# Kernel optimization log

Hardware: AMD Instinct MI355X
Metric: run time of the kernel (lower is better)

## Reference

```python
import jax, jax.numpy as jnp
import numpy as np

B, T, C, H = 8, 2048, 1024, 64  # batch, seq (== block_size), n_embd, head_size


def setup_inputs() -> dict:
    key = jax.random.key(0)
    k1, k2, k3, k4 = jax.random.split(key, 4)
    x = jax.random.normal(k1, (B, T, C), dtype=jnp.float32)
    scale = 0.02
    Wk = jax.random.normal(k2, (H, C), dtype=jnp.float32) * scale  # nn.Linear weight [out,in]
    Wq = jax.random.normal(k3, (H, C), dtype=jnp.float32) * scale
    Wv = jax.random.normal(k4, (H, C), dtype=jnp.float32) * scale
    return {"x": x, "Wk": Wk, "Wq": Wq, "Wv": Wv}


def reference(x, Wk, Wq, Wv):
    # k, q, v projections (bias-free linears): x @ W.T
    k = jnp.einsum('btc,hc->bth', x, Wk)
    q = jnp.einsum('btc,hc->bth', x, Wq)
    v = jnp.einsum('btc,hc->bth', x, Wv)
    # NOTE: source MULTIPLIES by sqrt(head_size) (faithful to original code)
    wei = jnp.einsum('bth,bsh->bts', q, k) * (H ** 0.5)  # [B,T,T]
    causal = jnp.tril(jnp.ones((T, T), dtype=bool))
    wei = jnp.where(causal, wei, -jnp.inf)
    wei = jax.nn.softmax(wei, axis=-1)
    # dropout_value = 0.0 -> identity (deterministic baseline)
    out = jnp.einsum('bts,bsh->bth', wei, v)  # [B,T,H]
    return out
```

## Files before the change

### kernel.cpp

```cpp
#include <hip/hip_runtime.h>

#define BB 8
#define TT 2048
#define CC 1024
#define HH 64
#define MM (BB * TT)

typedef _Float16 half8 __attribute__((ext_vector_type(8)));
typedef _Float16 half4 __attribute__((ext_vector_type(4)));
typedef float floatx4 __attribute__((ext_vector_type(4)));

template <int CTRL>
__device__ __forceinline__ float dpp_max_step(float x)
{
    union { float f; int i; } u, v;
    u.f = x;
    v.i = __builtin_amdgcn_update_dpp(u.i, u.i, CTRL, 0xf, 0xf, false);
    return fmaxf(x, v.f);
}
__device__ __forceinline__ float rowmax16(float x)
{
    x = dpp_max_step<0x128>(x);
    x = dpp_max_step<0x124>(x);
    x = dpp_max_step<0x122>(x);
    x = dpp_max_step<0x121>(x);
    return x;
}

__global__ __launch_bounds__(256)
void w_pack(const float* __restrict__ Wk, const float* __restrict__ Wq,
            const float* __restrict__ Wv, _Float16* __restrict__ Wp)
{
    const int idx = (blockIdx.x * 256 + threadIdx.x) * 8;
    const int c   = idx / 6144;
    const int rm  = idx - c * 6144;
    const int row = rm >> 5;
    const int kk  = rm & 31;
    const int which = row >> 6;
    const float* __restrict__ src = (which == 0) ? Wq : ((which == 1) ? Wk : Wv);
    const float scale = (which == 0) ? 8.0f : 1.0f;
    const int srow = row & 63;
    const int k = c * 32 + kk;
    const float4 a = *reinterpret_cast<const float4*>(&src[srow * 1024 + k]);
    const float4 b = *reinterpret_cast<const float4*>(&src[srow * 1024 + k + 4]);
    const half8 o = { (_Float16)(a.x * scale), (_Float16)(a.y * scale),
                      (_Float16)(a.z * scale), (_Float16)(a.w * scale),
                      (_Float16)(b.x * scale), (_Float16)(b.y * scale),
                      (_Float16)(b.z * scale), (_Float16)(b.w * scale) };
    *reinterpret_cast<half8*>(&Wp[idx]) = o;
}

__global__ __launch_bounds__(64, 2)
void qkv7(const float* __restrict__ x, const _Float16* __restrict__ Wp,
          _Float16* __restrict__ q16, _Float16* __restrict__ Kp,
          _Float16* __restrict__ Vp)
{
    const int lane  = threadIdx.x;
    const int gw    = blockIdx.x;
    const int mtile = gw >> 1;
    const int nh    = gw & 1;
    const int m_base = mtile * 16;
    const int fm = lane & 15;
    const int fq = lane >> 4;
    const int fk = fq * 8;
    const int fr = fq * 4;

    const float*    __restrict__ xrow = &x[(size_t)(m_base + fm) * CC + fk];
    const _Float16* __restrict__ wb   = &Wp[(nh * 96 + fm) * 32 + fk];

    floatx4 acc[6];
    #pragma unroll
    for (int n = 0; n < 6; ++n)
        #pragma unroll
        for (int r = 0; r < 4; ++r) acc[n][r] = 0.0f;

    float4 xa, xb, nxa, nxb;
    half8 wf[6], nwf[6];

    xa = *reinterpret_cast<const float4*>(xrow);
    xb = *reinterpret_cast<const float4*>(xrow + 4);
    #pragma unroll
    for (int n = 0; n < 6; ++n)
        wf[n] = *reinterpret_cast<const half8*>(wb + n * 512);

    #pragma unroll 2
    for (int c = 0; c < 32; ++c) {
        if (c < 31) {
            const float* xp = xrow + (c + 1) * 32;
            nxa = *reinterpret_cast<const float4*>(xp);
            nxb = *reinterpret_cast<const float4*>(xp + 4);
            const _Float16* wc = wb + (c + 1) * 6144;
            #pragma unroll
            for (int n = 0; n < 6; ++n)
                nwf[n] = *reinterpret_cast<const half8*>(wc + n * 512);
        }
        const half8 af = { (_Float16)xa.x, (_Float16)xa.y, (_Float16)xa.z, (_Float16)xa.w,
                           (_Float16)xb.x, (_Float16)xb.y, (_Float16)xb.z, (_Float16)xb.w };
        #pragma unroll
        for (int n = 0; n < 6; ++n)
            acc[n] = __builtin_amdgcn_mfma_f32_16x16x32_f16(af, wf[n], acc[n], 0, 0, 0);
        xa = nxa; xb = nxb;
        #pragma unroll
        for (int n = 0; n < 6; ++n) wf[n] = nwf[n];
    }

    #pragma unroll
    for (int n = 0; n < 6; ++n) {
        const int col = nh * 96 + n * 16 + fm;
        if (col < 64) {
            #pragma unroll
            for (int r = 0; r < 4; ++r)
                q16[(size_t)(m_base + fr + r) * HH + col] = (_Float16)acc[n][r];
        } else if (col < 128) {
            const int h = col - 64;
            _Float16* kp = &Kp[(size_t)(mtile * 2 + (h >> 5)) * 512 + (h & 31)];
            #pragma unroll
            for (int r = 0; r < 4; ++r)
                kp[(fr + r) * 32] = (_Float16)acc[n][r];
        } else {
            const int h = col - 128;
            const half4 pk = { (_Float16)acc[n][0], (_Float16)acc[n][1],
                               (_Float16)acc[n][2], (_Float16)acc[n][3] };
            *reinterpret_cast<half4*>(
                &Vp[(size_t)((mtile >> 2) * 4 + (h >> 4)) * 1024 +
                    ((mtile >> 1) & 1) * 512 + fm * 32 + (mtile & 1) * 16 + fr]) = pk;
        }
    }
}

__global__ __launch_bounds__(64, 4)
void attn7(const _Float16* __restrict__ q16, const _Float16* __restrict__ Kp,
           const _Float16* __restrict__ Vp, float* __restrict__ out,
           _Float16* __restrict__ Op, float* __restrict__ ml)
{
    __shared__ _Float16 Ps[16 * 68];

    const int bid = blockIdx.x;
    const int it  = 127 - bid / 24;
    const int sub = bid - (127 - it) * 24;
    const int b   = sub & 7;
    const int s   = sub >> 3;

    const int lane = threadIdx.x;
    const int fm = lane & 15;
    const int fq = lane >> 4;
    const int fk = fq * 8;
    const int fr = fq * 4;

    const int Ji = (it >> 2) + 1;
    const int qq = Ji / 3, rem = Ji - qq * 3;
    const int cnt   = qq + (s < rem ? 1 : 0);
    const int start = s * qq + (s < rem ? s : rem);

    const _Float16* __restrict__ kpb = Kp + (size_t)b * TT * HH;
    const _Float16* __restrict__ vpb = Vp + (size_t)b * TT * HH;

    const int qrow = (b * 128 + it) * 16 + fm;
    const half8 qf0 = *reinterpret_cast<const half8*>(&q16[(size_t)qrow * HH + fk]);
    const half8 qf1 = *reinterpret_cast<const half8*>(&q16[(size_t)qrow * HH + 32 + fk]);

    floatx4 O[4], lacc;
    float m_r[4];
    #pragma unroll
    for (int r = 0; r < 4; ++r) {
        m_r[r] = -3.0e38f;
        lacc[r] = 0.0f;
        #pragma unroll
        for (int ht = 0; ht < 4; ++ht) O[ht][r] = 0.0f;
    }
    const half8 ones = { (_Float16)1.f, (_Float16)1.f, (_Float16)1.f, (_Float16)1.f,
                         (_Float16)1.f, (_Float16)1.f, (_Float16)1.f, (_Float16)1.f };

    const int loff = fm * 32 + fk;

    for (int js = 0; js < cnt; ++js) {
        const int jj = start + js;

        floatx4 sa[4];
        #pragma unroll
        for (int nt = 0; nt < 4; ++nt) {
            #pragma unroll
            for (int r = 0; r < 4; ++r) sa[nt][r] = 0.0f;
            const _Float16* kp = &kpb[(size_t)(jj * 4 + nt) * 1024];
            const half8 b0 = *reinterpret_cast<const half8*>(kp + loff);
            const half8 b1 = *reinterpret_cast<const half8*>(kp + 512 + loff);
            sa[nt] = __builtin_amdgcn_mfma_f32_16x16x32_f16(qf0, b0, sa[nt], 0, 0, 0);
            sa[nt] = __builtin_amdgcn_mfma_f32_16x16x32_f16(qf1, b1, sa[nt], 0, 0, 0);
        }

        if (jj == (it >> 2)) {
            const int rbase = it * 16 + fr;
            #pragma unroll
            for (int nt = 0; nt < 4; ++nt) {
                const int col = jj * 64 + nt * 16 + fm;
                #pragma unroll
                for (int r = 0; r < 4; ++r)
                    if (col > rbase + r) sa[nt][r] = -3.0e38f;
            }
        }

        #pragma unroll
        for (int r = 0; r < 4; ++r) {
            float mx = fmaxf(fmaxf(sa[0][r], sa[1][r]), fmaxf(sa[2][r], sa[3][r]));
            mx = rowmax16(mx);
            const float mn = fmaxf(m_r[r], mx);
            const float alpha = __expf(m_r[r] - mn);
            m_r[r] = mn;
            _Float16* pp = &Ps[(fr + r) * 68 + fm];
            pp[0]  = (_Float16)__expf(sa[0][r] - mn);
            pp[16] = (_Float16)__expf(sa[1][r] - mn);
            pp[32] = (_Float16)__expf(sa[2][r] - mn);
            pp[48] = (_Float16)__expf(sa[3][r] - mn);
            lacc[r] *= alpha;
            O[0][r] *= alpha; O[1][r] *= alpha; O[2][r] *= alpha; O[3][r] *= alpha;
        }

        #pragma unroll
        for (int ch = 0; ch < 2; ++ch) {
            const half8 pa = *reinterpret_cast<const half8*>(&Ps[fm * 68 + ch * 32 + fk]);
            lacc = __builtin_amdgcn_mfma_f32_16x16x32_f16(pa, ones, lacc, 0, 0, 0);
            #pragma unroll
            for (int ht = 0; ht < 4; ++ht) {
                const half8 vb = *reinterpret_cast<const half8*>(
                    &vpb[(size_t)(jj * 4 + ht) * 1024 + ch * 512 + loff]);
                O[ht] = __builtin_amdgcn_mfma_f32_16x16x32_f16(pa, vb, O[ht], 0, 0, 0);
            }
        }
    }

    #pragma unroll
    for (int r = 0; r < 4; ++r) {
        const int grow = (b * 128 + it) * 16 + fr + r;
        if (s == 0) {
            #pragma unroll
            for (int ht = 0; ht < 4; ++ht)
                out[(size_t)grow * HH + ht * 16 + fm] = O[ht][r];
        } else {
            #pragma unroll
            for (int ht = 0; ht < 4; ++ht)
                Op[((size_t)(s - 1) * MM + grow) * HH + ht * 16 + fm] = (_Float16)O[ht][r];
        }
        if (fm == 0) {
            ml[((size_t)s * MM + grow) * 2 + 0] = m_r[r];
            ml[((size_t)s * MM + grow) * 2 + 1] = lacc[r];
        }
    }
}

__global__ __launch_bounds__(256)
void combine(float* __restrict__ out, const _Float16* __restrict__ Op,
             const float* __restrict__ ml)
{
    const int tid  = threadIdx.x;
    const int grow = blockIdx.x * 64 + (tid >> 2);
    const int c0   = (tid & 3) * 16;

    const float m0 = ml[(size_t)grow * 2 + 0];
    const float l0 = ml[(size_t)grow * 2 + 1];
    const float m1 = ml[((size_t)MM + grow) * 2 + 0];
    const float l1 = ml[((size_t)MM + grow) * 2 + 1];
    const float m2 = ml[((size_t)2 * MM + grow) * 2 + 0];
    const float l2 = ml[((size_t)2 * MM + grow) * 2 + 1];

    const float M  = fmaxf(m0, fmaxf(m1, m2));
    const float w0 = __expf(m0 - M);
    const float w1 = __expf(m1 - M);
    const float w2 = __expf(m2 - M);
    const float inv = 1.0f / (w0 * l0 + w1 * l1 + w2 * l2);

    #pragma unroll
    for (int i = 0; i < 16; i += 4) {
        float4 o0 = *reinterpret_cast<float4*>(&out[(size_t)grow * HH + c0 + i]);
        const half4 h1 = *reinterpret_cast<const half4*>(&Op[(size_t)grow * HH + c0 + i]);
        const half4 h2 = *reinterpret_cast<const half4*>(&Op[(size_t)MM * HH + (size_t)grow * HH + c0 + i]);
        o0.x = (w0 * o0.x + w1 * (float)h1[0] + w2 * (float)h2[0]) * inv;
        o0.y = (w0 * o0.y + w1 * (float)h1[1] + w2 * (float)h2[1]) * inv;
        o0.z = (w0 * o0.z + w1 * (float)h1[2] + w2 * (float)h2[2]) * inv;
        o0.w = (w0 * o0.w + w1 * (float)h1[3] + w2 * (float)h2[3]) * inv;
        *reinterpret_cast<float4*>(&out[(size_t)grow * HH + c0 + i]) = o0;
    }
}

extern "C" void kernel_launch(void* const* d_in, const int* in_sizes, int n_in,
                              void* d_out, int out_size, void* d_ws, size_t ws_size,
                              hipStream_t stream)
{
    (void)in_sizes; (void)n_in; (void)out_size; (void)ws_size;

    const float* x  = (const float*)d_in[0];
    const float* Wk = (const float*)d_in[1];
    const float* Wq = (const float*)d_in[2];
    const float* Wv = (const float*)d_in[3];
    float* out = (float*)d_out;

    _Float16* base = (_Float16*)d_ws;
    _Float16* q16 = base;
    _Float16* Kp  = base + (size_t)MM * HH;
    _Float16* Vp  = base + (size_t)2 * MM * HH;
    _Float16* Wp  = base + (size_t)3 * MM * HH;
    _Float16* Op  = Wp + 192 * 1024;
    float*    ml  = (float*)(Op + (size_t)2 * MM * HH);

    w_pack<<<dim3(96), dim3(256), 0, stream>>>(Wk, Wq, Wv, Wp);
    qkv7<<<dim3(2048), dim3(64), 0, stream>>>(x, Wp, q16, Kp, Vp);
    attn7<<<dim3(3072), dim3(64), 0, stream>>>(q16, Kp, Vp, out, Op, ml);
    combine<<<dim3(256), dim3(256), 0, stream>>>(out, Op, ml);
}
```

Measured before the change: 151.0 us.

## Use 4-wave blocks with LDS-staged, swizzled K/V and x tiles via async global-to-LDS loads

Both the QKV projection and attention kernels now run 256-thread blocks of four waves. Each block shares K/V (attention) or x (projection) tiles staged in double-buffered LDS through global_load_lds. Packed K/V layouts are rewritten with an XOR swizzle to avoid LDS bank conflicts. Before, each wave read K/V fragments straight from global memory for its own 16-row query tile, so the same K/V data was fetched repeatedly across waves. The new scheme adds __syncthreads per step, raises LDS usage, and coarsens the split-K work units, which can hurt load balance across the causal triangle.

Result: no change. 153.3 us (+1.5%).

```diff
diff --git a/kernel.cpp b/kernel.cpp
--- a/kernel.cpp
+++ b/kernel.cpp
@@ -9,6 +9,13 @@
 typedef _Float16 half8 __attribute__((ext_vector_type(8)));
 typedef _Float16 half4 __attribute__((ext_vector_type(4)));
 typedef float floatx4 __attribute__((ext_vector_type(4)));
+
+__device__ __forceinline__ void gload_lds16(const void* g, void* l)
+{
+    __builtin_amdgcn_global_load_lds(
+        (const __attribute__((address_space(1))) unsigned int*)g,
+        (__attribute__((address_space(3))) unsigned int*)l, 16, 0, 0);
+}
 
 template <int CTRL>
 __device__ __forceinline__ float dpp_max_step(float x)
@@ -50,23 +57,28 @@
     *reinterpret_cast<half8*>(&Wp[idx]) = o;
 }
 
-__global__ __launch_bounds__(64, 2)
-void qkv7(const float* __restrict__ x, const _Float16* __restrict__ Wp,
+__global__ __launch_bounds__(256, 3)
+void qkv8(const float* __restrict__ x, const _Float16* __restrict__ Wp,
           _Float16* __restrict__ q16, _Float16* __restrict__ Kp,
           _Float16* __restrict__ Vp)
 {
-    const int lane  = threadIdx.x;
-    const int gw    = blockIdx.x;
-    const int mtile = gw >> 1;
-    const int nh    = gw & 1;
-    const int m_base = mtile * 16;
+    __shared__ float Xs[2][64 * 32];
+
+    const int tid  = threadIdx.x;
+    const int lane = tid & 63;
+    const int wv   = tid >> 6;
+    const int m_base = (blockIdx.x >> 1) * 64;
+    const int nbase  = (blockIdx.x & 1) * 96;
     const int fm = lane & 15;
     const int fq = lane >> 4;
     const int fk = fq * 8;
     const int fr = fq * 4;
 
-    const float*    __restrict__ xrow = &x[(size_t)(m_base + fm) * CC + fk];
-    const _Float16* __restrict__ wb   = &Wp[(nh * 96 + fm) * 32 + fk];
+    const int srow = wv * 16 + (lane >> 3);
+    const int gg   = (lane & 7) ^ (lane >> 3);
+    const float* __restrict__ gx0 = &x[(size_t)(m_base + srow) * CC + gg * 4];
+
+    const _Float16* __restrict__ wbase = &Wp[(nbase + fm) * 32 + fk];
 
     floatx4 acc[6];
     #pragma unroll
@@ -74,88 +86,108 @@
         #pragma unroll
         for (int r = 0; r < 4; ++r) acc[n][r] = 0.0f;
 
-    float4 xa, xb, nxa, nxb;
-    half8 wf[6], nwf[6];
-
-    xa = *reinterpret_cast<const float4*>(xrow);
-    xb = *reinterpret_cast<const float4*>(xrow + 4);
+    half8 wf[6], wfn[6];
+
+    gload_lds16(gx0,            &Xs[0][(wv * 2 + 0) * 256]);
+    gload_lds16(gx0 + 8 * CC,   &Xs[0][(wv * 2 + 1) * 256]);
     #pragma unroll
     for (int n = 0; n < 6; ++n)
-        wf[n] = *reinterpret_cast<const half8*>(wb + n * 512);
-
-    #pragma unroll 2
+        wf[n] = *reinterpret_cast<const half8*>(wbase + n * 512);
+
+    const int arow = wv * 16 + fm;
+    const int p0 = ((2 * fq) ^ (fm & 7)) * 4;
+    const int p1 = ((2 * fq + 1) ^ (fm & 7)) * 4;
+
     for (int c = 0; c < 32; ++c) {
-        if (c < 31) {
-            const float* xp = xrow + (c + 1) * 32;
-            nxa = *reinterpret_cast<const float4*>(xp);
-            nxb = *reinterpret_cast<const float4*>(xp + 4);
-            const _Float16* wc = wb + (c + 1) * 6144;
+        const int cur = c & 1;
+        __syncthreads();
+        if (c + 1 < 32) {
+            const float* gx = gx0 + (c + 1) * 32;
+            gload_lds16(gx,          &Xs[1 - cur][(wv * 2 + 0) * 256]);
+            gload_lds16(gx + 8 * CC, &Xs[1 - cur][(wv * 2 + 1) * 256]);
+            const _Float16* wc = wbase + (c + 1) * 6144;
             #pragma unroll
             for (int n = 0; n < 6; ++n)
-                nwf[n] = *reinterpret_cast<const half8*>(wc + n * 512);
-        }
-        const half8 af = { (_Float16)xa.x, (_Float16)xa.y, (_Float16)xa.z, (_Float16)xa.w,
-                           (_Float16)xb.x, (_Float16)xb.y, (_Float16)xb.z, (_Float16)xb.w };
+                wfn[n] = *reinterpret_cast<const half8*>(wc + n * 512);
+        }
+        const float4 a0 = *reinterpret_cast<const float4*>(&Xs[cur][arow * 32 + p0]);
+        const float4 a1 = *reinterpret_cast<const float4*>(&Xs[cur][arow * 32 + p1]);
+        const half8 af = { (_Float16)a0.x, (_Float16)a0.y, (_Float16)a0.z, (_Float16)a0.w,
+                           (_Float16)a1.x, (_Float16)a1.y, (_Float16)a1.z, (_Float16)a1.w };
         #pragma unroll
         for (int n = 0; n < 6; ++n)
             acc[n] = __builtin_amdgcn_mfma_f32_16x16x32_f16(af, wf[n], acc[n], 0, 0, 0);
-        xa = nxa; xb = nxb;
-        #pragma unroll
-        for (int n = 0; n < 6; ++n) wf[n] = nwf[n];
-    }
-
+        if (c + 1 < 32) {
+            #pragma unroll
+            for (int n = 0; n < 6; ++n) wf[n] = wfn[n];
+        }
+    }
+
+    const size_t bt = (size_t)(m_base >> 6) * 8;
     #pragma unroll
     for (int n = 0; n < 6; ++n) {
-        const int col = nh * 96 + n * 16 + fm;
+        const int col = nbase + n * 16 + fm;
         if (col < 64) {
             #pragma unroll
             for (int r = 0; r < 4; ++r)
-                q16[(size_t)(m_base + fr + r) * HH + col] = (_Float16)acc[n][r];
+                q16[(size_t)(m_base + wv * 16 + fr + r) * HH + col] = (_Float16)acc[n][r];
         } else if (col < 128) {
             const int h = col - 64;
-            _Float16* kp = &Kp[(size_t)(mtile * 2 + (h >> 5)) * 512 + (h & 31)];
-            #pragma unroll
-            for (int r = 0; r < 4; ++r)
-                kp[(fr + r) * 32] = (_Float16)acc[n][r];
+            const int f = wv * 2 + (h >> 5);
+            const int j = h & 7;
+            #pragma unroll
+            for (int r = 0; r < 4; ++r) {
+                const int kl = fr + r;
+                const int g  = kl * 4 + ((h & 31) >> 3);
+                const int sg = g ^ ((g >> 3) & 7);
+                Kp[(bt + f) * 512 + sg * 8 + j] = (_Float16)acc[n][r];
+            }
         } else {
-            const int h = col - 128;
+            const int h   = col - 128;
+            const int klq = wv * 16 + fr;
+            const int f   = (h >> 4) * 2 + (klq >> 5);
+            const int g   = (h & 15) * 4 + ((klq & 31) >> 3);
+            const int sg  = g ^ ((g >> 3) & 7);
+            const int j0  = klq & 7;
             const half4 pk = { (_Float16)acc[n][0], (_Float16)acc[n][1],
                                (_Float16)acc[n][2], (_Float16)acc[n][3] };
-            *reinterpret_cast<half4*>(
-                &Vp[(size_t)((mtile >> 2) * 4 + (h >> 4)) * 1024 +
-                    ((mtile >> 1) & 1) * 512 + fm * 32 + (mtile & 1) * 16 + fr]) = pk;
-        }
-    }
-}
-
-__global__ __launch_bounds__(64, 4)
-void attn7(const _Float16* __restrict__ q16, const _Float16* __restrict__ Kp,
+            *reinterpret_cast<half4*>(&Vp[(bt + f) * 512 + sg * 8 + j0]) = pk;
+        }
+    }
+}
+
+__global__ __launch_bounds__(256, 3)
+void attn8(const _Float16* __restrict__ q16, const _Float16* __restrict__ Kp,
            const _Float16* __restrict__ Vp, float* __restrict__ out,
            _Float16* __restrict__ Op, float* __restrict__ ml)
 {
-    __shared__ _Float16 Ps[16 * 68];
+    __shared__ _Float16 Kb[2][8 * 512];
+    __shared__ _Float16 Vb[2][8 * 512];
+    __shared__ _Float16 Ps[4][16 * 68];
 
     const int bid = blockIdx.x;
-    const int it  = 127 - bid / 24;
-    const int sub = bid - (127 - it) * 24;
+    const int it  = 31 - bid / 24;
+    const int sub = bid - (31 - it) * 24;
     const int b   = sub & 7;
     const int s   = sub >> 3;
 
-    const int lane = threadIdx.x;
+    const int tid  = threadIdx.x;
+    const int lane = tid & 63;
+    const int wv   = tid >> 6;
     const int fm = lane & 15;
     const int fq = lane >> 4;
     const int fk = fq * 8;
     const int fr = fq * 4;
 
-    const int Ji = (it >> 2) + 1;
+    const int Ji = it + 1;
     const int qq = Ji / 3, rem = Ji - qq * 3;
     const int cnt   = qq + (s < rem ? 1 : 0);
     const int start = s * qq + (s < rem ? s : rem);
 
-    const _Float16* __restrict__ kpb = Kp + (size_t)b * TT * HH;
-    const _Float16* __restrict__ vpb = Vp + (size_t)b * TT * HH;
-
-    const int qrow = (b * 128 + it) * 16 + fm;
+    const _Float16* __restrict__ kpb = Kp + (size_t)(b * 32) * 4096;
+    const _Float16* __restrict__ vpb = Vp + (size_t)(b * 32) * 4096;
+
+    const int qrow = b * TT + it * 64 + wv * 16 + fm;
     const half8 qf0 = *reinterpret_cast<const half8*>(&q16[(size_t)qrow * HH + fk]);
     const half8 qf1 = *reinterpret_cast<const half8*>(&q16[(size_t)qrow * HH + 32 + fk]);
 
@@ -171,25 +203,42 @@
     const half8 ones = { (_Float16)1.f, (_Float16)1.f, (_Float16)1.f, (_Float16)1.f,
                          (_Float16)1.f, (_Float16)1.f, (_Float16)1.f, (_Float16)1.f };
 
-    const int loff = fm * 32 + fk;
+    const int gQ = fm * 4 + fq;
+    const int pQ = (gQ ^ ((gQ >> 3) & 7)) * 8;
+
+    if (cnt > 0) {
+        const size_t tb = (size_t)start * 4096;
+        gload_lds16(kpb + tb + (2 * wv + 0) * 512 + lane * 8, &Kb[0][(2 * wv + 0) * 512]);
+        gload_lds16(kpb + tb + (2 * wv + 1) * 512 + lane * 8, &Kb[0][(2 * wv + 1) * 512]);
+        gload_lds16(vpb + tb + (2 * wv + 0) * 512 + lane * 8, &Vb[0][(2 * wv + 0) * 512]);
+        gload_lds16(vpb + tb + (2 * wv + 1) * 512 + lane * 8, &Vb[0][(2 * wv + 1) * 512]);
+    }
 
     for (int js = 0; js < cnt; ++js) {
-        const int jj = start + js;
+        const int jj  = start + js;
+        const int cur = js & 1;
+        __syncthreads();
+        if (js + 1 < cnt) {
+            const size_t tb = (size_t)(jj + 1) * 4096;
+            gload_lds16(kpb + tb + (2 * wv + 0) * 512 + lane * 8, &Kb[1 - cur][(2 * wv + 0) * 512]);
+            gload_lds16(kpb + tb + (2 * wv + 1) * 512 + lane * 8, &Kb[1 - cur][(2 * wv + 1) * 512]);
+            gload_lds16(vpb + tb + (2 * wv + 0) * 512 + lane * 8, &Vb[1 - cur][(2 * wv + 0) * 512]);
+            gload_lds16(vpb + tb + (2 * wv + 1) * 512 + lane * 8, &Vb[1 - cur][(2 * wv + 1) * 512]);
+        }
 
         floatx4 sa[4];
         #pragma unroll
         for (int nt = 0; nt < 4; ++nt) {
             #pragma unroll
             for (int r = 0; r < 4; ++r) sa[nt][r] = 0.0f;
-            const _Float16* kp = &kpb[(size_t)(jj * 4 + nt) * 1024];
-            const half8 b0 = *reinterpret_cast<const half8*>(kp + loff);
-            const half8 b1 = *reinterpret_cast<const half8*>(kp + 512 + loff);
+            const half8 b0 = *reinterpret_cast<const half8*>(&Kb[cur][(nt * 2 + 0) * 512 + pQ]);
+            const half8 b1 = *reinterpret_cast<const half8*>(&Kb[cur][(nt * 2 + 1) * 512 + pQ]);
             sa[nt] = __builtin_amdgcn_mfma_f32_16x16x32_f16(qf0, b0, sa[nt], 0, 0, 0);
             sa[nt] = __builtin_amdgcn_mfma_f32_16x16x32_f16(qf1, b1, sa[nt], 0, 0, 0);
         }
 
-        if (jj == (it >> 2)) {
-            const int rbase = it * 16 + fr;
+        if (jj == it) {
+            const int rbase = it * 64 + wv * 16 + fr;
             #pragma unroll
             for (int nt = 0; nt < 4; ++nt) {
                 const int col = jj * 64 + nt * 16 + fm;
@@ -206,7 +255,7 @@
             const float mn = fmaxf(m_r[r], mx);
             const float alpha = __expf(m_r[r] - mn);
             m_r[r] = mn;
-            _Float16* pp = &Ps[(fr + r) * 68 + fm];
+            _Float16* pp = &Ps[wv][(fr + r) * 68 + fm];
             pp[0]  = (_Float16)__expf(sa[0][r] - mn);
             pp[16] = (_Float16)__expf(sa[1][r] - mn);
             pp[32] = (_Float16)__expf(sa[2][r] - mn);
@@ -217,20 +266,19 @@
 
         #pragma unroll
         for (int ch = 0; ch < 2; ++ch) {
-            const half8 pa = *reinterpret_cast<const half8*>(&Ps[fm * 68 + ch * 32 + fk]);
+            const half8 pa = *reinterpret_cast<const half8*>(&Ps[wv][fm * 68 + ch * 32 + fk]);
             lacc = __builtin_amdgcn_mfma_f32_16x16x32_f16(pa, ones, lacc, 0, 0, 0);
             #pragma unroll
             for (int ht = 0; ht < 4; ++ht) {
-                const half8 vb = *reinterpret_cast<const half8*>(
-                    &vpb[(size_t)(jj * 4 + ht) * 1024 + ch * 512 + loff]);
-                O[ht] = __builtin_amdgcn_mfma_f32_16x16x32_f16(pa, vb, O[ht], 0, 0, 0);
+                const half8 vbf = *reinterpret_cast<const half8*>(&Vb[cur][(ht * 2 + ch) * 512 + pQ]);
+                O[ht] = __builtin_amdgcn_mfma_f32_16x16x32_f16(pa, vbf, O[ht], 0, 0, 0);
             }
         }
     }
 
     #pragma unroll
     for (int r = 0; r < 4; ++r) {
-        const int grow = (b * 128 + it) * 16 + fr + r;
+        const int grow = b * TT + it * 64 + wv * 16 + fr + r;
         if (s == 0) {
             #pragma unroll
             for (int ht = 0; ht < 4; ++ht)
@@ -302,7 +350,7 @@
     float*    ml  = (float*)(Op + (size_t)2 * MM * HH);
 
     w_pack<<<dim3(96), dim3(256), 0, stream>>>(Wk, Wq, Wv, Wp);
-    qkv7<<<dim3(2048), dim3(64), 0, stream>>>(x, Wp, q16, Kp, Vp);
-    attn7<<<dim3(3072), dim3(64), 0, stream>>>(q16, Kp, Vp, out, Op, ml);
+    qkv8<<<dim3(512), dim3(256), 0, stream>>>(x, Wp, q16, Kp, Vp);
+    attn8<<<dim3(768), dim3(256), 0, stream>>>(q16, Kp, Vp, out, Op, ml);
     combine<<<dim3(256), dim3(256), 0, stream>>>(out, Op, ml);
 }
```
